# Performance work log

Hardware: AMD Instinct MI355X
Metric: run time of the kernel (lower is better)

## Reference

```python
import jax, jax.numpy as jnp
import numpy as np

N = 8192      # reg_num == number of nodes
E = 524288    # number of edges
OUT = 32      # out_num


def gcn_conv(x, src, dst, W, b, n):
    """PyG GCNConv: add self-loops, symmetric deg^-1/2 normalization, linear, scatter-add, bias."""
    loop = jnp.arange(n)
    s = jnp.concatenate([src, loop])
    d = jnp.concatenate([dst, loop])
    deg = jax.ops.segment_sum(jnp.ones(s.shape, dtype=x.dtype), d, num_segments=n)
    dinv = jnp.where(deg > 0, jax.lax.rsqrt(deg), jnp.zeros_like(deg))
    norm = dinv[s] * dinv[d]                      # [E+N]
    h = x @ W.T                                    # [N, out_ch]
    out = jax.ops.segment_sum(norm[:, None] * h[s], d, num_segments=n)
    return out + b


def setup_inputs() -> dict:
    key = jax.random.key(0)
    ks = jax.random.split(key, 12)
    data = jax.random.normal(ks[0], (N, 2), dtype=jnp.float32)
    edge = jax.random.randint(ks[1], (2, E), 0, N, dtype=jnp.int64)
    # GCNConv weights (PyG Linear: y = x @ W.T, bias added after aggregation)
    W1 = jax.random.normal(ks[2], (4, 2), dtype=jnp.float32) * 0.5
    b1 = jnp.zeros((4,), dtype=jnp.float32)
    W2 = jax.random.normal(ks[3], (2, 4), dtype=jnp.float32) * 0.5
    b2 = jnp.zeros((2,), dtype=jnp.float32)
    W3 = jax.random.normal(ks[4], (1, 2), dtype=jnp.float32) * 0.5
    b3 = jnp.zeros((1,), dtype=jnp.float32)
    # trailing MLP: Linear(N, 2N) -> Tanh -> Linear(2N, OUT) -> Tanh
    Wa = jax.random.normal(ks[5], (2 * N, N), dtype=jnp.float32) * (1.0 / np.sqrt(N))
    ba = jnp.zeros((2 * N,), dtype=jnp.float32)
    Wb = jax.random.normal(ks[6], (OUT, 2 * N), dtype=jnp.float32) * (1.0 / np.sqrt(2 * N))
    bb = jnp.zeros((OUT,), dtype=jnp.float32)
    return {"data": data, "edge": edge, "W1": W1, "b1": b1, "W2": W2, "b2": b2,
            "W3": W3, "b3": b3, "Wa": Wa, "ba": ba, "Wb": Wb, "bb": bb}


def reference(data, edge, W1, b1, W2, b2, W3, b3, Wa, ba, Wb, bb):
    src, dst = edge[0], edge[1]
    n = data.shape[0]
    out = jax.nn.relu(gcn_conv(data, src, dst, W1, b1, n))
    out = jax.nn.relu(gcn_conv(out, src, dst, W2, b2, n))
    out = gcn_conv(out, src, dst, W3, b3, n)       # [N, 1]
    out = out.reshape(1, -1)                        # [1, N]
    out = jnp.tanh(out @ Wa.T + ba)                 # [1, 2N]
    out = jnp.tanh(out @ Wb.T + bb)                 # [1, OUT]
    return out
```

## Files before the change

kernel.cpp:

```cpp
#include <hip/hip_runtime.h>
#include <hip/hip_bf16.h>

#define NN   8192
#define NE   524288
#define DH   16384
#define NOUT 32

typedef float f32x4 __attribute__((ext_vector_type(4)));


__global__ __launch_bounds__(256) void k_hist(const int* __restrict__ dst, int* cnt) {
    int e = blockIdx.x * blockDim.x + threadIdx.x;
    if (e < NE) atomicAdd(&cnt[dst[e]], 1);
}

__global__ __launch_bounds__(256) void k_scan(const int* __restrict__ cnt,
                                              int* __restrict__ row,
                                              int* __restrict__ cursor,
                                              float* __restrict__ dinv) {
    __shared__ int sm[256];
    int t = threadIdx.x;
    int base = t * 32;
    int local[32];
    int sum = 0;
#pragma unroll
    for (int k = 0; k < 32; ++k) { local[k] = cnt[base + k]; sum += local[k]; }
    sm[t] = sum;
    __syncthreads();
    for (int off = 1; off < 256; off <<= 1) {
        int v = (t >= off) ? sm[t - off] : 0;
        __syncthreads();
        sm[t] += v;
        __syncthreads();
    }
    int pre = (t == 0) ? 0 : sm[t - 1];
#pragma unroll
    for (int k = 0; k < 32; ++k) {
        row[base + k] = pre;
        cursor[base + k] = pre;
        dinv[base + k] = rsqrtf((float)local[k] + 1.0f);
        pre += local[k];
    }
    if (t == 255) row[NN] = pre;
}

__global__ __launch_bounds__(256) void k_build(const int* __restrict__ src,
                                               const int* __restrict__ dst,
                                               int* __restrict__ cursor,
                                               int* __restrict__ srcs) {
    int e = blockIdx.x * blockDim.x + threadIdx.x;
    if (e >= NE) return;
    int p = atomicAdd(&cursor[dst[e]], 1);
    srcs[p] = src[e];
}

__global__ __launch_bounds__(256) void k_h1(const float* __restrict__ x0,
                                            const float* __restrict__ W1,
                                            float* __restrict__ h1) {
    int i = blockIdx.x * blockDim.x + threadIdx.x;
    if (i >= NN) return;
    float a = x0[2 * i], b = x0[2 * i + 1];
    f32x4 h;
#pragma unroll
    for (int c = 0; c < 4; ++c) h[c] = a * W1[2 * c] + b * W1[2 * c + 1];
    *(f32x4*)(h1 + 4 * i) = h;
}


__global__ __launch_bounds__(256) void k_g4(const int* __restrict__ row,
                                            const int* __restrict__ srcs,
                                            const float* __restrict__ dinv,
                                            const float* __restrict__ h1,
                                            const float* __restrict__ b1,
                                            const float* __restrict__ W2,
                                            float* __restrict__ h2) {
    int wid = threadIdx.x >> 6, lane = threadIdx.x & 63;
    int i = blockIdx.x * 4 + wid;
    int beg = row[i], end = row[i + 1];
    float a0 = 0, a1 = 0, a2 = 0, a3 = 0;
    for (int p = beg + lane; p < end; p += 64) {
        int s = srcs[p];
        float w = dinv[s];
        float4 hv = *(const float4*)(h1 + 4 * s);
        a0 += w * hv.x; a1 += w * hv.y; a2 += w * hv.z; a3 += w * hv.w;
    }
#pragma unroll
    for (int off = 32; off > 0; off >>= 1) {
        a0 += __shfl_down(a0, off, 64);
        a1 += __shfl_down(a1, off, 64);
        a2 += __shfl_down(a2, off, 64);
        a3 += __shfl_down(a3, off, 64);
    }
    if (lane == 0) {
        float di = dinv[i];
        float4 hs = *(const float4*)(h1 + 4 * i);
        float x0v = fmaxf(di * (a0 + di * hs.x) + b1[0], 0.0f);
        float x1v = fmaxf(di * (a1 + di * hs.y) + b1[1], 0.0f);
        float x2v = fmaxf(di * (a2 + di * hs.z) + b1[2], 0.0f);
        float x3v = fmaxf(di * (a3 + di * hs.w) + b1[3], 0.0f);
        float2 o;
        o.x = x0v * W2[0] + x1v * W2[1] + x2v * W2[2] + x3v * W2[3];
        o.y = x0v * W2[4] + x1v * W2[5] + x2v * W2[6] + x3v * W2[7];
        *(float2*)(h2 + 2 * i) = o;
    }
}

__global__ __launch_bounds__(256) void k_g2(const int* __restrict__ row,
                                            const int* __restrict__ srcs,
                                            const float* __restrict__ dinv,
                                            const float* __restrict__ h2,
                                            const float* __restrict__ b2,
                                            const float* __restrict__ W3,
                                            float* __restrict__ h3) {
    int wid = threadIdx.x >> 6, lane = threadIdx.x & 63;
    int i = blockIdx.x * 4 + wid;
    int beg = row[i], end = row[i + 1];
    float a0 = 0, a1 = 0;
    for (int p = beg + lane; p < end; p += 64) {
        int s = srcs[p];
        float w = dinv[s];
        float2 hv = *(const float2*)(h2 + 2 * s);
        a0 += w * hv.x; a1 += w * hv.y;
    }
#pragma unroll
    for (int off = 32; off > 0; off >>= 1) {
        a0 += __shfl_down(a0, off, 64);
        a1 += __shfl_down(a1, off, 64);
    }
    if (lane == 0) {
        float di = dinv[i];
        float2 hs = *(const float2*)(h2 + 2 * i);
        float x0v = fmaxf(di * (a0 + di * hs.x) + b2[0], 0.0f);
        float x1v = fmaxf(di * (a1 + di * hs.y) + b2[1], 0.0f);
        h3[i] = x0v * W3[0] + x1v * W3[1];
    }
}

__global__ __launch_bounds__(256) void k_g1(const int* __restrict__ row,
                                            const int* __restrict__ srcs,
                                            const float* __restrict__ dinv,
                                            const float* __restrict__ h3,
                                            const float* __restrict__ b3,
                                            float* __restrict__ v) {
    int wid = threadIdx.x >> 6, lane = threadIdx.x & 63;
    int i = blockIdx.x * 4 + wid;
    int beg = row[i], end = row[i + 1];
    float a0 = 0;
    for (int p = beg + lane; p < end; p += 64) {
        int s = srcs[p];
        a0 += dinv[s] * h3[s];
    }
#pragma unroll
    for (int off = 32; off > 0; off >>= 1) a0 += __shfl_down(a0, off, 64);
    if (lane == 0) {
        float di = dinv[i];
        v[i] = di * (a0 + di * h3[i]) + b3[0];
    }
}


__global__ __launch_bounds__(256) void k_mv1(const float* __restrict__ v,
                                             const float* __restrict__ Wa,
                                             const float* __restrict__ ba,
                                             float* __restrict__ y) {
    int wid  = threadIdx.x >> 6;
    int lane = threadIdx.x & 63;
    int j = blockIdx.x * 4 + wid;
    const f32x4* wr = (const f32x4*)(Wa + (size_t)j * NN);
    const f32x4* vv = (const f32x4*)v;
    float acc = 0.0f;
#pragma unroll 8
    for (int it = 0; it < (NN / 4) / 64; ++it) {
        int idx = it * 64 + lane;
        f32x4 w = __builtin_nontemporal_load(&wr[idx]);
        f32x4 x = vv[idx];
        acc += w.x * x.x + w.y * x.y + w.z * x.z + w.w * x.w;
    }
#pragma unroll
    for (int off = 32; off > 0; off >>= 1) acc += __shfl_down(acc, off, 64);
    if (lane == 0) y[j] = tanhf(acc + ba[j]);
}

__global__ __launch_bounds__(256) void k_mv2(const float* __restrict__ y,
                                             const float* __restrict__ Wb,
                                             const float* __restrict__ bb,
                                             float* __restrict__ out) {
    int wid  = threadIdx.x >> 6;
    int lane = threadIdx.x & 63;
    int o = blockIdx.x * 4 + wid;
    const f32x4* wr = (const f32x4*)(Wb + (size_t)o * DH);
    const f32x4* yy = (const f32x4*)y;
    float acc = 0.0f;
#pragma unroll 8
    for (int it = 0; it < (DH / 4) / 64; ++it) {
        int idx = it * 64 + lane;
        f32x4 w = wr[idx];
        f32x4 x = yy[idx];
        acc += w.x * x.x + w.y * x.y + w.z * x.z + w.w * x.w;
    }
#pragma unroll
    for (int off = 32; off > 0; off >>= 1) acc += __shfl_down(acc, off, 64);
    if (lane == 0) out[o] = tanhf(acc + bb[o]);
}


extern "C" void kernel_launch(void* const* d_in, const int* in_sizes, int n_in,
                              void* d_out, int out_size, void* d_ws, size_t ws_size,
                              hipStream_t stream) {
    const float* data = (const float*)d_in[0];
    const int*   edge = (const int*)d_in[1];
    const float* W1   = (const float*)d_in[2];
    const float* b1   = (const float*)d_in[3];
    const float* W2   = (const float*)d_in[4];
    const float* b2   = (const float*)d_in[5];
    const float* W3   = (const float*)d_in[6];
    const float* b3   = (const float*)d_in[7];
    const float* Wa   = (const float*)d_in[8];
    const float* ba   = (const float*)d_in[9];
    const float* Wb   = (const float*)d_in[10];
    const float* bb   = (const float*)d_in[11];
    float* out = (float*)d_out;

    const int* src = edge;
    const int* dst = edge + NE;

    char* ws = (char*)d_ws;
    int*   cnt    = (int*)ws;
    int*   row    = cnt + NN;
    int*   cursor = row + NN + 1;
    int*   srcs   = cursor + NN;
    float* dinv   = (float*)(srcs + NE);
    float* h1     = dinv + NN;
    float* h2     = h1 + NN * 4;
    float* h3     = h2 + NN * 2;
    float* v      = h3 + NN;
    float* y1     = v + NN;

    dim3 blk(256);
    dim3 gN((NN + 255) / 256);
    dim3 gE((NE + 255) / 256);
    dim3 gW(NN / 4);

    hipMemsetAsync(cnt, 0, (size_t)NN * sizeof(int), stream);

    k_hist <<<gE, blk, 0, stream>>>(dst, cnt);
    k_h1   <<<gN, blk, 0, stream>>>(data, W1, h1);
    k_scan <<<dim3(1), blk, 0, stream>>>(cnt, row, cursor, dinv);
    k_build<<<gE, blk, 0, stream>>>(src, dst, cursor, srcs);
    k_g4   <<<gW, blk, 0, stream>>>(row, srcs, dinv, h1, b1, W2, h2);
    k_g2   <<<gW, blk, 0, stream>>>(row, srcs, dinv, h2, b2, W3, h3);
    k_g1   <<<gW, blk, 0, stream>>>(row, srcs, dinv, h3, b3, v);
    k_mv1  <<<dim3(DH / 4), blk, 0, stream>>>(v, Wa, ba, y1);
    k_mv2  <<<dim3(NOUT / 4), blk, 0, stream>>>(y1, Wb, bb, out);
}
```

Baseline: 747.6 us.

## Fuse GCN graph-build and three aggregation layers into one cooperative kernel

```diff
diff --git a/kernel.cpp b/kernel.cpp
--- a/kernel.cpp
+++ b/kernel.cpp
@@ -1,160 +1,163 @@
 #include <hip/hip_runtime.h>
 #include <hip/hip_bf16.h>
+#include <hip/hip_cooperative_groups.h>
+
+namespace cg = cooperative_groups;
 
 #define NN   8192
 #define NE   524288
 #define DH   16384
 #define NOUT 32
 
+#define NBLK 1024
+#define NTHR 256
+#define NT   (NBLK * NTHR)
+#define NWAVE (NBLK * 4)
+
 typedef float f32x4 __attribute__((ext_vector_type(4)));
 
 
-__global__ __launch_bounds__(256) void k_hist(const int* __restrict__ dst, int* cnt) {
-    int e = blockIdx.x * blockDim.x + threadIdx.x;
-    if (e < NE) atomicAdd(&cnt[dst[e]], 1);
-}
-
-__global__ __launch_bounds__(256) void k_scan(const int* __restrict__ cnt,
-                                              int* __restrict__ row,
-                                              int* __restrict__ cursor,
-                                              float* __restrict__ dinv) {
-    __shared__ int sm[256];
-    int t = threadIdx.x;
-    int base = t * 32;
-    int local[32];
-    int sum = 0;
-#pragma unroll
-    for (int k = 0; k < 32; ++k) { local[k] = cnt[base + k]; sum += local[k]; }
-    sm[t] = sum;
-    __syncthreads();
-    for (int off = 1; off < 256; off <<= 1) {
-        int v = (t >= off) ? sm[t - off] : 0;
+__global__ __launch_bounds__(256, 4) void k_gcn(
+    const float* __restrict__ data,
+    const float* __restrict__ W1, const float* __restrict__ b1,
+    const float* __restrict__ W2, const float* __restrict__ b2,
+    const float* __restrict__ W3, const float* __restrict__ b3,
+    const int* __restrict__ src, const int* __restrict__ dst,
+    int* cnt, int* row, int* cursor, int* srcs,
+    float* dinv, float* h1, float* h2, float* h3, float* v)
+{
+    cg::grid_group grid = cg::this_grid();
+    const int tid  = blockIdx.x * NTHR + threadIdx.x;
+    const int wid  = threadIdx.x >> 6;
+    const int lane = threadIdx.x & 63;
+    const int gw   = blockIdx.x * 4 + wid;
+
+    if (tid < NN) {
+        cnt[tid] = 0;
+        float a = data[2 * tid], b = data[2 * tid + 1];
+        float4 h;
+        h.x = a * W1[0] + b * W1[1];
+        h.y = a * W1[2] + b * W1[3];
+        h.z = a * W1[4] + b * W1[5];
+        h.w = a * W1[6] + b * W1[7];
+        *(float4*)(h1 + 4 * tid) = h;
+    }
+    const int e0 = tid, e1 = tid + NT;
+    const int d0 = dst[e0], d1 = dst[e1];
+    grid.sync();
+
+    atomicAdd(&cnt[d0], 1);
+    atomicAdd(&cnt[d1], 1);
+    grid.sync();
+
+    if (blockIdx.x == 0) {
+        __shared__ int sm[256];
+        int t = threadIdx.x, base = t * 32;
+        int local[32], sum = 0;
+#pragma unroll
+        for (int k = 0; k < 32; ++k) { local[k] = cnt[base + k]; sum += local[k]; }
+        sm[t] = sum;
         __syncthreads();
-        sm[t] += v;
-        __syncthreads();
-    }
-    int pre = (t == 0) ? 0 : sm[t - 1];
-#pragma unroll
-    for (int k = 0; k < 32; ++k) {
-        row[base + k] = pre;
-        cursor[base + k] = pre;
-        dinv[base + k] = rsqrtf((float)local[k] + 1.0f);
-        pre += local[k];
-    }
-    if (t == 255) row[NN] = pre;
-}
-
-__global__ __launch_bounds__(256) void k_build(const int* __restrict__ src,
-                                               const int* __restrict__ dst,
-                                               int* __restrict__ cursor,
-                                               int* __restrict__ srcs) {
-    int e = blockIdx.x * blockDim.x + threadIdx.x;
-    if (e >= NE) return;
-    int p = atomicAdd(&cursor[dst[e]], 1);
-    srcs[p] = src[e];
-}
-
-__global__ __launch_bounds__(256) void k_h1(const float* __restrict__ x0,
-                                            const float* __restrict__ W1,
-                                            float* __restrict__ h1) {
-    int i = blockIdx.x * blockDim.x + threadIdx.x;
-    if (i >= NN) return;
-    float a = x0[2 * i], b = x0[2 * i + 1];
-    f32x4 h;
-#pragma unroll
-    for (int c = 0; c < 4; ++c) h[c] = a * W1[2 * c] + b * W1[2 * c + 1];
-    *(f32x4*)(h1 + 4 * i) = h;
-}
-
-
-__global__ __launch_bounds__(256) void k_g4(const int* __restrict__ row,
-                                            const int* __restrict__ srcs,
-                                            const float* __restrict__ dinv,
-                                            const float* __restrict__ h1,
-                                            const float* __restrict__ b1,
-                                            const float* __restrict__ W2,
-                                            float* __restrict__ h2) {
-    int wid = threadIdx.x >> 6, lane = threadIdx.x & 63;
-    int i = blockIdx.x * 4 + wid;
-    int beg = row[i], end = row[i + 1];
-    float a0 = 0, a1 = 0, a2 = 0, a3 = 0;
-    for (int p = beg + lane; p < end; p += 64) {
-        int s = srcs[p];
-        float w = dinv[s];
-        float4 hv = *(const float4*)(h1 + 4 * s);
-        a0 += w * hv.x; a1 += w * hv.y; a2 += w * hv.z; a3 += w * hv.w;
-    }
-#pragma unroll
-    for (int off = 32; off > 0; off >>= 1) {
-        a0 += __shfl_down(a0, off, 64);
-        a1 += __shfl_down(a1, off, 64);
-        a2 += __shfl_down(a2, off, 64);
-        a3 += __shfl_down(a3, off, 64);
-    }
-    if (lane == 0) {
-        float di = dinv[i];
-        float4 hs = *(const float4*)(h1 + 4 * i);
-        float x0v = fmaxf(di * (a0 + di * hs.x) + b1[0], 0.0f);
-        float x1v = fmaxf(di * (a1 + di * hs.y) + b1[1], 0.0f);
-        float x2v = fmaxf(di * (a2 + di * hs.z) + b1[2], 0.0f);
-        float x3v = fmaxf(di * (a3 + di * hs.w) + b1[3], 0.0f);
-        float2 o;
-        o.x = x0v * W2[0] + x1v * W2[1] + x2v * W2[2] + x3v * W2[3];
-        o.y = x0v * W2[4] + x1v * W2[5] + x2v * W2[6] + x3v * W2[7];
-        *(float2*)(h2 + 2 * i) = o;
-    }
-}
-
-__global__ __launch_bounds__(256) void k_g2(const int* __restrict__ row,
-                                            const int* __restrict__ srcs,
-                                            const float* __restrict__ dinv,
-                                            const float* __restrict__ h2,
-                                            const float* __restrict__ b2,
-                                            const float* __restrict__ W3,
-                                            float* __restrict__ h3) {
-    int wid = threadIdx.x >> 6, lane = threadIdx.x & 63;
-    int i = blockIdx.x * 4 + wid;
-    int beg = row[i], end = row[i + 1];
-    float a0 = 0, a1 = 0;
-    for (int p = beg + lane; p < end; p += 64) {
-        int s = srcs[p];
-        float w = dinv[s];
-        float2 hv = *(const float2*)(h2 + 2 * s);
-        a0 += w * hv.x; a1 += w * hv.y;
-    }
-#pragma unroll
-    for (int off = 32; off > 0; off >>= 1) {
-        a0 += __shfl_down(a0, off, 64);
-        a1 += __shfl_down(a1, off, 64);
-    }
-    if (lane == 0) {
-        float di = dinv[i];
-        float2 hs = *(const float2*)(h2 + 2 * i);
-        float x0v = fmaxf(di * (a0 + di * hs.x) + b2[0], 0.0f);
-        float x1v = fmaxf(di * (a1 + di * hs.y) + b2[1], 0.0f);
-        h3[i] = x0v * W3[0] + x1v * W3[1];
-    }
-}
-
-__global__ __launch_bounds__(256) void k_g1(const int* __restrict__ row,
-                                            const int* __restrict__ srcs,
-                                            const float* __restrict__ dinv,
-                                            const float* __restrict__ h3,
-                                            const float* __restrict__ b3,
-                                            float* __restrict__ v) {
-    int wid = threadIdx.x >> 6, lane = threadIdx.x & 63;
-    int i = blockIdx.x * 4 + wid;
-    int beg = row[i], end = row[i + 1];
-    float a0 = 0;
-    for (int p = beg + lane; p < end; p += 64) {
-        int s = srcs[p];
-        a0 += dinv[s] * h3[s];
-    }
-#pragma unroll
-    for (int off = 32; off > 0; off >>= 1) a0 += __shfl_down(a0, off, 64);
-    if (lane == 0) {
-        float di = dinv[i];
-        v[i] = di * (a0 + di * h3[i]) + b3[0];
+        for (int off = 1; off < 256; off <<= 1) {
+            int vv = (t >= off) ? sm[t - off] : 0;
+            __syncthreads();
+            sm[t] += vv;
+            __syncthreads();
+        }
+        int pre = (t == 0) ? 0 : sm[t - 1];
+#pragma unroll
+        for (int k = 0; k < 32; ++k) {
+            row[base + k] = pre;
+            cursor[base + k] = pre;
+            dinv[base + k] = rsqrtf((float)local[k] + 1.0f);
+            pre += local[k];
+        }
+        if (t == 255) row[NN] = pre;
+    }
+    grid.sync();
+
+    {
+        int s0 = src[e0], s1 = src[e1];
+        int p0 = atomicAdd(&cursor[d0], 1); srcs[p0] = s0;
+        int p1 = atomicAdd(&cursor[d1], 1); srcs[p1] = s1;
+    }
+    grid.sync();
+
+    const int i0 = gw, i1 = gw + NWAVE;
+    const int beg0 = row[i0], end0 = row[i0 + 1];
+    const int beg1 = row[i1], end1 = row[i1 + 1];
+
+#pragma unroll
+    for (int r = 0; r < 2; ++r) {
+        int i = r ? i1 : i0, beg = r ? beg1 : beg0, end = r ? end1 : end0;
+        float a0 = 0, a1 = 0, a2 = 0, a3 = 0;
+        for (int p = beg + lane; p < end; p += 64) {
+            int s = srcs[p];
+            float w = dinv[s];
+            float4 hv = *(const float4*)(h1 + 4 * s);
+            a0 += w * hv.x; a1 += w * hv.y; a2 += w * hv.z; a3 += w * hv.w;
+        }
+#pragma unroll
+        for (int off = 32; off > 0; off >>= 1) {
+            a0 += __shfl_down(a0, off, 64);
+            a1 += __shfl_down(a1, off, 64);
+            a2 += __shfl_down(a2, off, 64);
+            a3 += __shfl_down(a3, off, 64);
+        }
+        if (lane == 0) {
+            float di = dinv[i];
+            float4 hs = *(const float4*)(h1 + 4 * i);
+            float x0v = fmaxf(di * (a0 + di * hs.x) + b1[0], 0.0f);
+            float x1v = fmaxf(di * (a1 + di * hs.y) + b1[1], 0.0f);
+            float x2v = fmaxf(di * (a2 + di * hs.z) + b1[2], 0.0f);
+            float x3v = fmaxf(di * (a3 + di * hs.w) + b1[3], 0.0f);
+            float2 o;
+            o.x = x0v * W2[0] + x1v * W2[1] + x2v * W2[2] + x3v * W2[3];
+            o.y = x0v * W2[4] + x1v * W2[5] + x2v * W2[6] + x3v * W2[7];
+            *(float2*)(h2 + 2 * i) = o;
+        }
+    }
+    grid.sync();
+
+#pragma unroll
+    for (int r = 0; r < 2; ++r) {
+        int i = r ? i1 : i0, beg = r ? beg1 : beg0, end = r ? end1 : end0;
+        float a0 = 0, a1 = 0;
+        for (int p = beg + lane; p < end; p += 64) {
+            int s = srcs[p];
+            float w = dinv[s];
+            float2 hv = *(const float2*)(h2 + 2 * s);
+            a0 += w * hv.x; a1 += w * hv.y;
+        }
+#pragma unroll
+        for (int off = 32; off > 0; off >>= 1) {
+            a0 += __shfl_down(a0, off, 64);
+            a1 += __shfl_down(a1, off, 64);
+        }
+        if (lane == 0) {
+            float di = dinv[i];
+            float2 hs = *(const float2*)(h2 + 2 * i);
+            float x0v = fmaxf(di * (a0 + di * hs.x) + b2[0], 0.0f);
+            float x1v = fmaxf(di * (a1 + di * hs.y) + b2[1], 0.0f);
+            h3[i] = x0v * W3[0] + x1v * W3[1];
+        }
+    }
+    grid.sync();
+
+#pragma unroll
+    for (int r = 0; r < 2; ++r) {
+        int i = r ? i1 : i0, beg = r ? beg1 : beg0, end = r ? end1 : end0;
+        float a0 = 0;
+        for (int p = beg + lane; p < end; p += 64) {
+            int s = srcs[p];
+            a0 += dinv[s] * h3[s];
+        }
+#pragma unroll
+        for (int off = 32; off > 0; off >>= 1) a0 += __shfl_down(a0, off, 64);
+        if (lane == 0) {
+            float di = dinv[i];
+            v[i] = di * (a0 + di * h3[i]) + b3[0];
+        }
     }
 }
 
@@ -236,20 +239,15 @@
     float* v      = h3 + NN;
     float* y1     = v + NN;
 
-    dim3 blk(256);
-    dim3 gN((NN + 255) / 256);
-    dim3 gE((NE + 255) / 256);
-    dim3 gW(NN / 4);
-
-    hipMemsetAsync(cnt, 0, (size_t)NN * sizeof(int), stream);
-
-    k_hist <<<gE, blk, 0, stream>>>(dst, cnt);
-    k_h1   <<<gN, blk, 0, stream>>>(data, W1, h1);
-    k_scan <<<dim3(1), blk, 0, stream>>>(cnt, row, cursor, dinv);
-    k_build<<<gE, blk, 0, stream>>>(src, dst, cursor, srcs);
-    k_g4   <<<gW, blk, 0, stream>>>(row, srcs, dinv, h1, b1, W2, h2);
-    k_g2   <<<gW, blk, 0, stream>>>(row, srcs, dinv, h2, b2, W3, h3);
-    k_g1   <<<gW, blk, 0, stream>>>(row, srcs, dinv, h3, b3, v);
-    k_mv1  <<<dim3(DH / 4), blk, 0, stream>>>(v, Wa, ba, y1);
-    k_mv2  <<<dim3(NOUT / 4), blk, 0, stream>>>(y1, Wb, bb, out);
-}
+    void* args[] = {
+        (void*)&data, (void*)&W1, (void*)&b1, (void*)&W2, (void*)&b2,
+        (void*)&W3, (void*)&b3, (void*)&src, (void*)&dst,
+        (void*)&cnt, (void*)&row, (void*)&cursor, (void*)&srcs,
+        (void*)&dinv, (void*)&h1, (void*)&h2, (void*)&h3, (void*)&v
+    };
+    hipLaunchCooperativeKernel((const void*)k_gcn, dim3(NBLK), dim3(NTHR),
+                               args, 0, stream);
+
+    k_mv1<<<dim3(DH / 4), dim3(256), 0, stream>>>(v, Wa, ba, y1);
+    k_mv2<<<dim3(NOUT / 4), dim3(256), 0, stream>>>(y1, Wb, bb, out);
+}
```

New measurement: 1.413 ms. 1.89x slower.
